# Kernel optimization log

Hardware: AMD Instinct MI355X
Metric: run time of the kernel (lower is better)

## Reference

```python
import jax, jax.numpy as jnp
import numpy as np

N_NODES = 50000
IN_CH, HID_CH, OUT_CH = 256, 128, 64
N_EDGES = 800000


def setup_inputs() -> dict:
    key = jax.random.key(0)
    ks = jax.random.split(key, 8)
    x = jax.random.normal(ks[0], (N_NODES, IN_CH), dtype=jnp.float32)
    edge_index = jax.random.randint(ks[1], (2, N_EDGES), 0, N_NODES, dtype=jnp.int64)
    edge_weight = jax.random.uniform(ks[2], (N_EDGES,), dtype=jnp.float32)
    # Glorot-style init for the two GCNConv linear layers (PyG uses glorot init, zero bias)
    W1 = jax.random.normal(ks[3], (IN_CH, HID_CH), dtype=jnp.float32) * (2.0 / (IN_CH + HID_CH)) ** 0.5
    b1 = jnp.zeros((HID_CH,), dtype=jnp.float32)
    W2 = jax.random.normal(ks[4], (HID_CH, OUT_CH), dtype=jnp.float32) * (2.0 / (HID_CH + OUT_CH)) ** 0.5
    b2 = jnp.zeros((OUT_CH,), dtype=jnp.float32)
    return {"x": x, "edge_index": edge_index, "edge_weight": edge_weight,
            "W1": W1, "b1": b1, "W2": W2, "b2": b2}


def _gcn_norm(edge_index, edge_weight, num_nodes):
    # PyG gcn_norm with add_self_loops=True: append self loops (weight 1.0),
    # deg[j] = sum of incoming edge weights, norm_e = deg[src]^-1/2 * w_e * deg[dst]^-1/2
    loop = jnp.arange(num_nodes, dtype=edge_index.dtype)
    row = jnp.concatenate([edge_index[0], loop])  # source nodes
    col = jnp.concatenate([edge_index[1], loop])  # destination nodes
    w = jnp.concatenate([edge_weight, jnp.ones((num_nodes,), dtype=edge_weight.dtype)])
    deg = jax.ops.segment_sum(w, col, num_segments=num_nodes)  # [N]
    deg_inv_sqrt = jnp.where(deg > 0, jax.lax.rsqrt(jnp.where(deg > 0, deg, 1.0)), 0.0)
    norm = deg_inv_sqrt[row] * w * deg_inv_sqrt[col]  # [E+N]
    return row, col, norm


def _gcn_conv(x, W, b, row, col, norm, num_nodes):
    h = x @ W                              # [N, C_out] dense linear first (as in PyG)
    msg = h[row] * norm[:, None]           # gather + per-edge scale: [E+N, C_out]
    out = jax.ops.segment_sum(msg, col, num_segments=num_nodes)  # scatter-add to dst
    return out + b


def reference(x, edge_index, edge_weight, W1, b1, W2, b2):
    num_nodes = x.shape[0]
    row, col, norm = _gcn_norm(edge_index, edge_weight, num_nodes)
    h = _gcn_conv(x, W1, b1, row, col, norm, num_nodes)
    h = jax.nn.relu(h)
    # dropout p=0.2 is identity in eval mode (training=False)
    out = _gcn_conv(h, W2, b2, row, col, norm, num_nodes)
    return out
```

## Files before the change

kernel.cpp:

```cpp
#include <hip/hip_runtime.h>
#include <hip/hip_bf16.h>
#include <math.h>

static constexpr int NNODES = 50000;
static constexpr int NEDGES = 800000;
static constexpr int NBUCK = (NNODES + 255) >> 8;
static constexpr int MAXB = 6144;

typedef __attribute__((ext_vector_type(8))) short bf16x8;
typedef __attribute__((ext_vector_type(4))) float f32x4;

__device__ inline short f2bf(float f) {
  union { __hip_bfloat16 h; short s; } u;
  u.h = __float2bfloat16(f);
  return u.s;
}

__device__ inline float bf2f(short s) {
  union { unsigned int u; float f; } u;
  u.u = ((unsigned int)(unsigned short)s) << 16;
  return u.f;
}

__device__ inline void i8x8_to_f32(uint2 v, float* f) {
#pragma unroll
  for (int j = 0; j < 4; ++j) f[j] = (float)(signed char)((v.x >> (8 * j)) & 0xFF);
#pragma unroll
  for (int j = 0; j < 4; ++j) f[4 + j] = (float)(signed char)((v.y >> (8 * j)) & 0xFF);
}


template <int K, int NTOT>
__device__ inline void packW_body(const float* __restrict__ W, short* __restrict__ Wpk, int t) {
  constexpr int KF = K / 32;
  constexpr int NPF = NTOT / 16;
  if (t >= KF * NPF * 64) return;
  int f = t >> 6, l = t & 63;
  int kf = f / NPF, nfb = f % NPF;
  int col = nfb * 16 + (l & 15);
  int krow = kf * 32 + (l >> 4) * 8;
  bf16x8 bv;
#pragma unroll
  for (int i = 0; i < 8; ++i) bv[i] = f2bf(W[(size_t)(krow + i) * NTOT + col]);
  ((bf16x8*)Wpk)[t] = bv;
}

__global__ void setup_kernel(const float* __restrict__ W1, short* __restrict__ Wpk1,
                             const float* __restrict__ W2, short* __restrict__ Wpk2,
                             int* __restrict__ gcur) {
  const int bid = blockIdx.x, tid = threadIdx.x;
  if (bid < 16) {
    packW_body<256, 128>(W1, Wpk1, bid * 256 + tid);
  } else if (bid < 20) {
    packW_body<128, 64>(W2, Wpk2, (bid - 16) * 256 + tid);
  } else {
    if (tid < NBUCK) gcur[tid] = tid * MAXB;
  }
}


__global__ __launch_bounds__(256) void bin_kernel(const int* __restrict__ row,
                                                  const int* __restrict__ col,
                                                  const float* __restrict__ w,
                                                  int* __restrict__ gcur,
                                                  int2* __restrict__ binned, int e_cnt) {
  __shared__ int rcnt[NBUCK];
  __shared__ int rcur[NBUCK];
  __shared__ int gbase[NBUCK];
  const int tid = threadIdx.x;
  for (int b = tid; b < NBUCK; b += 256) {
    rcnt[b] = 0;
    rcur[b] = 0;
  }
  __syncthreads();
  const int base = blockIdx.x * 2048;
  int srcs[8], dsts[8];
  float ws_[8];
#pragma unroll
  for (int j = 0; j < 8; ++j) {
    int idx = base + tid + 256 * j;
    if (idx < e_cnt) {
      srcs[j] = row[idx];
      dsts[j] = col[idx];
      ws_[j] = w[idx];
      atomicAdd(&rcnt[dsts[j] >> 8], 1);
    } else {
      dsts[j] = -1;
    }
  }
  __syncthreads();
  for (int b = tid; b < NBUCK; b += 256)
    if (rcnt[b] > 0) gbase[b] = atomicAdd(&gcur[b], rcnt[b]);
  __syncthreads();
#pragma unroll
  for (int j = 0; j < 8; ++j) {
    if (dsts[j] >= 0) {
      int b = dsts[j] >> 8;
      int dl = dsts[j] & 255;
      int pos = gbase[b] + atomicAdd(&rcur[b], 1);
      binned[pos] = make_int2((dl << 16) | srcs[j], __float_as_int(ws_[j]));
    }
  }
}

__global__ __launch_bounds__(256) void bdeg_kernel(const int2* __restrict__ binned,
                                                   const int* __restrict__ gcur,
                                                   float* __restrict__ dinv,
                                                   int* __restrict__ cntg,
                                                   int* __restrict__ bbase, int n) {
  const int b = blockIdx.x, tid = threadIdx.x;
  if (b == NBUCK) {
    __shared__ int buf[256];
    int v = (tid < NBUCK) ? gcur[tid] - tid * MAXB : 0;
    buf[tid] = v;
    __syncthreads();
    for (int off = 1; off < 256; off <<= 1) {
      int t = (tid >= off) ? buf[tid - off] : 0;
      __syncthreads();
      buf[tid] += t;
      __syncthreads();
    }
    if (tid < NBUCK) bbase[tid] = buf[tid] - v;
    return;
  }
  __shared__ float degf[256];
  __shared__ int cnt[256];
  degf[tid] = 0.f;
  cnt[tid] = 0;
  __syncthreads();
  const int bcnt = gcur[b] - b * MAXB;
  const int2* bp = binned + (size_t)b * MAXB;
  for (int i = tid; i < bcnt; i += 256) {
    int2 e = bp[i];
    int dl = (e.x >> 16) & 255;
    atomicAdd(&degf[dl], __int_as_float(e.y));
    atomicAdd(&cnt[dl], 1);
  }
  __syncthreads();
  int node = b * 256 + tid;
  if (node < n) {
    dinv[node] = 1.0f / sqrtf(degf[tid] + 1.0f);
    cntg[node] = cnt[tid];
  }
}

__global__ __launch_bounds__(256) void csrfill_kernel(
    const int2* __restrict__ binned, const int* __restrict__ gcur,
    const int* __restrict__ bbase, const float* __restrict__ dinv,
    const int* __restrict__ cntg, int* __restrict__ start,
    unsigned int* __restrict__ csr, int n) {
  __shared__ float dvL[256];
  __shared__ int cur[256];
  __shared__ int buf[256];
  const int b = blockIdx.x, tid = threadIdx.x;
  const int node = b * 256 + tid;
  int c = (node < n) ? cntg[node] : 0;
  dvL[tid] = (node < n) ? dinv[node] : 0.f;
  buf[tid] = c;
  __syncthreads();
  for (int off = 1; off < 256; off <<= 1) {
    int t = (tid >= off) ? buf[tid - off] : 0;
    __syncthreads();
    buf[tid] += t;
    __syncthreads();
  }
  int localstart = buf[tid] - c;
  const int gb = bbase[b];
  if (node < n) start[node] = gb + localstart;
  cur[tid] = localstart;
  __syncthreads();
  const int bcnt = gcur[b] - b * MAXB;
  const int2* bp = binned + (size_t)b * MAXB;
  for (int i = tid; i < bcnt; i += 256) {
    int2 e = bp[i];
    int src = e.x & 0xFFFF;
    int dl = (e.x >> 16) & 255;
    float nrm = dinv[src] * __int_as_float(e.y) * dvL[dl];
    int pos = gb + atomicAdd(&cur[dl], 1);
    csr[pos] = (unsigned int)src | ((unsigned int)(unsigned short)f2bf(nrm) << 16);
  }
}


template <int K, int NTOT, bool A_BF16>
__global__ __launch_bounds__(64, 4) void mfma_gemm_kernel(const void* __restrict__ Av,
                                                          const short* __restrict__ Wpk,
                                                          unsigned char* __restrict__ H,
                                                          float* __restrict__ sc, int n) {
  constexpr int KF = K / 32;
  constexpr int NF = NTOT / 16;
  const int lane = threadIdx.x;
  const int lrow = lane & 15;
  const int lgrp = lane >> 4;
  const int rowbase = blockIdx.x * 16;
  const int nmax = n - 1;
  int r = rowbase + lrow;
  r = r > nmax ? nmax : r;
  const bf16x8* Wf = (const bf16x8*)Wpk;
  f32x4 acc[NF] = {};

#pragma unroll
  for (int ks = 0; ks < KF; ++ks) {
    bf16x8 a;
    if (A_BF16) {
      const short* X = (const short*)Av;
      a = *(const bf16x8*)(X + (size_t)r * K + ks * 32 + lgrp * 8);
    } else {
      const float* X = (const float*)Av;
      const float* xp = X + (size_t)r * K + ks * 32 + lgrp * 8;
      float4 x0 = *(const float4*)xp;
      float4 x1 = *(const float4*)(xp + 4);
      a[0] = f2bf(x0.x);
      a[1] = f2bf(x0.y);
      a[2] = f2bf(x0.z);
      a[3] = f2bf(x0.w);
      a[4] = f2bf(x1.x);
      a[5] = f2bf(x1.y);
      a[6] = f2bf(x1.z);
      a[7] = f2bf(x1.w);
    }
#pragma unroll
    for (int nf = 0; nf < NF; ++nf) {
      bf16x8 bfr = Wf[(ks * NF + nf) * 64 + lane];
      acc[nf] = __builtin_amdgcn_mfma_f32_16x16x32_bf16(a, bfr, acc[nf], 0, 0, 0);
    }
  }

#pragma unroll
  for (int rr = 0; rr < 4; ++rr) {
    float m = 0.f;
#pragma unroll
    for (int nf = 0; nf < NF; ++nf) m = fmaxf(m, fabsf(acc[nf][rr]));
#pragma unroll
    for (int mask = 1; mask <= 8; mask <<= 1) m = fmaxf(m, __shfl_xor(m, mask));
    const int r2 = rowbase + lgrp * 4 + rr;
    const float inv = (m > 0.f) ? 127.f / m : 0.f;
    if (lrow == 0) sc[r2] = m * (1.f / 127.f);
#pragma unroll
    for (int nf = 0; nf < NF; ++nf) {
      int qv = (int)rintf(acc[nf][rr] * inv);
      qv = qv > 127 ? 127 : (qv < -127 ? -127 : qv);
      H[(size_t)r2 * NTOT + nf * 16 + lrow] = (unsigned char)(signed char)qv;
    }
  }
}


template <int CH, int TPN, bool RELU, bool OUT_BF16>
__global__ __launch_bounds__(256) void gatherq_kernel(
    const unsigned char* __restrict__ h, const float* __restrict__ sc,
    const float* __restrict__ dinv, const float* __restrict__ b,
    const int* __restrict__ start, const unsigned int* __restrict__ csr,
    void* __restrict__ outp, int n, int e_cnt) {
  constexpr int NPB = 256 / TPN;
  const int tid = threadIdx.x;
  const int q = tid % TPN;
  const int g = tid / TPN;
  const int d = blockIdx.x * NPB + g;
  if (d >= n) return;
  float s = dinv[d];
  s = s * s * sc[d];
  float f[8];
  i8x8_to_f32(*(const uint2*)(h + (size_t)d * CH + q * 8), f);
  float a0[8], a1[8], a2[8], a3[8];
#pragma unroll
  for (int j = 0; j < 8; ++j) {
    a0[j] = f[j] * s + b[q * 8 + j];
    a1[j] = 0.f;
    a2[j] = 0.f;
    a3[j] = 0.f;
  }
  const int k0 = start[d];
  const int k1 = (d + 1 < n) ? start[d + 1] : e_cnt;
  int k = k0;
  for (; k + 4 <= k1; k += 4) {
    unsigned int e0 = csr[k];
    unsigned int e1 = csr[k + 1];
    unsigned int e2 = csr[k + 2];
    unsigned int e3 = csr[k + 3];
    const int s0 = e0 & 0xFFFF, s1 = e1 & 0xFFFF, s2 = e2 & 0xFFFF, s3 = e3 & 0xFFFF;
    uint2 v0 = *(const uint2*)(h + (size_t)s0 * CH + q * 8);
    uint2 v1 = *(const uint2*)(h + (size_t)s1 * CH + q * 8);
    uint2 v2 = *(const uint2*)(h + (size_t)s2 * CH + q * 8);
    uint2 v3 = *(const uint2*)(h + (size_t)s3 * CH + q * 8);
    float n0 = bf2f((short)(e0 >> 16)) * sc[s0];
    float n1 = bf2f((short)(e1 >> 16)) * sc[s1];
    float n2 = bf2f((short)(e2 >> 16)) * sc[s2];
    float n3 = bf2f((short)(e3 >> 16)) * sc[s3];
    i8x8_to_f32(v0, f);
#pragma unroll
    for (int j = 0; j < 8; ++j) a0[j] += f[j] * n0;
    i8x8_to_f32(v1, f);
#pragma unroll
    for (int j = 0; j < 8; ++j) a1[j] += f[j] * n1;
    i8x8_to_f32(v2, f);
#pragma unroll
    for (int j = 0; j < 8; ++j) a2[j] += f[j] * n2;
    i8x8_to_f32(v3, f);
#pragma unroll
    for (int j = 0; j < 8; ++j) a3[j] += f[j] * n3;
  }
  for (; k < k1; ++k) {
    unsigned int e = csr[k];
    const int s0 = e & 0xFFFF;
    float nv = bf2f((short)(e >> 16)) * sc[s0];
    i8x8_to_f32(*(const uint2*)(h + (size_t)s0 * CH + q * 8), f);
#pragma unroll
    for (int j = 0; j < 8; ++j) a0[j] += f[j] * nv;
  }
#pragma unroll
  for (int j = 0; j < 8; ++j) a0[j] += (a1[j] + a2[j]) + a3[j];
  if (RELU) {
#pragma unroll
    for (int j = 0; j < 8; ++j) a0[j] = fmaxf(a0[j], 0.f);
  }
  if (OUT_BF16) {
    bf16x8 ov;
#pragma unroll
    for (int j = 0; j < 8; ++j) ov[j] = f2bf(a0[j]);
    *(bf16x8*)((short*)outp + (size_t)d * CH + q * 8) = ov;
  } else {
    float4* op = (float4*)outp + ((size_t)d * CH + q * 8) / 4;
    op[0] = make_float4(a0[0], a0[1], a0[2], a0[3]);
    op[1] = make_float4(a0[4], a0[5], a0[6], a0[7]);
  }
}


extern "C" void kernel_launch(void* const* d_in, const int* in_sizes, int n_in,
                              void* d_out, int out_size, void* d_ws, size_t ws_size,
                              hipStream_t stream) {
  const float* x = (const float*)d_in[0];
  const int* ei = (const int*)d_in[1];
  const float* ew = (const float*)d_in[2];
  const float* W1 = (const float*)d_in[3];
  const float* b1 = (const float*)d_in[4];
  const float* W2 = (const float*)d_in[5];
  const float* b2 = (const float*)d_in[6];
  float* outp = (float*)d_out;

  const int N = NNODES, E = NEDGES;
  const int* rowp = ei;
  const int* colp = ei + E;

  char* wsb = (char*)d_ws;
  int2* binned = (int2*)wsb;        wsb += (size_t)NBUCK * MAXB * 8;
  unsigned int* csr = (unsigned int*)wsb;  wsb += (size_t)E * 4;
  short* h1r = (short*)wsb;         wsb += (size_t)N * 128 * 2;
  unsigned char* h1 = (unsigned char*)wsb; wsb += (size_t)N * 128;
  unsigned char* h2 = (unsigned char*)wsb; wsb += (size_t)N * 64;
  short* Wpk1 = (short*)wsb;        wsb += (size_t)256 * 128 * 2;
  short* Wpk2 = (short*)wsb;        wsb += (size_t)128 * 64 * 2;
  float* sc1 = (float*)wsb;         wsb += (size_t)N * 4;
  float* sc2 = (float*)wsb;         wsb += (size_t)N * 4;
  float* dinv = (float*)wsb;        wsb += (size_t)N * 4;
  int* start = (int*)wsb;           wsb += (size_t)N * 4;
  int* cntg = (int*)wsb;            wsb += (size_t)N * 4;
  int* gcur = (int*)wsb;            wsb += (size_t)NBUCK * 4;
  int* bbase = (int*)wsb;           wsb += (size_t)NBUCK * 4;

  setup_kernel<<<21, 256, 0, stream>>>(W1, Wpk1, W2, Wpk2, gcur);

  bin_kernel<<<(E + 2047) / 2048, 256, 0, stream>>>(rowp, colp, ew, gcur, binned, E);
  bdeg_kernel<<<NBUCK + 1, 256, 0, stream>>>(binned, gcur, dinv, cntg, bbase, N);
  csrfill_kernel<<<NBUCK, 256, 0, stream>>>(binned, gcur, bbase, dinv, cntg, start, csr, N);

  mfma_gemm_kernel<256, 128, false><<<(N + 15) / 16, 64, 0, stream>>>(x, Wpk1, h1, sc1, N);
  gatherq_kernel<128, 16, true, true><<<(N + 15) / 16, 256, 0, stream>>>(
      h1, sc1, dinv, b1, start, csr, h1r, N, E);

  mfma_gemm_kernel<128, 64, true><<<(N + 15) / 16, 64, 0, stream>>>(h1r, Wpk2, h2, sc2, N);
  gatherq_kernel<64, 8, false, false><<<(N + 31) / 32, 256, 0, stream>>>(
      h2, sc2, dinv, b2, start, csr, outp, N, E);
}
```

Baseline: 108.2 us.

## Fuse first GEMM with edge binning into one heterogeneous kernel launch

Merges the layer-1 MFMA GEMM and the edge-binning pass into a single launch. Block IDs below a threshold run the GEMM, with four waves per block each handling 16 rows. The remaining blocks do binning, now processing 4096 edges per workgroup instead of 2048. This removes a launch and lets the independent GEMM and binning work run concurrently on the GPU. The cost is that the binning blocks reserve shared memory for bucket counters even on the GEMM path, and each binning thread holds more registers, which could lower occupancy.

```diff
diff --git a/kernel.cpp b/kernel.cpp
--- a/kernel.cpp
+++ b/kernel.cpp
@@ -6,6 +6,8 @@
 static constexpr int NEDGES = 800000;
 static constexpr int NBUCK = (NNODES + 255) >> 8;
 static constexpr int MAXB = 6144;
+static constexpr int GEMM1_BLKS = (NNODES + 63) / 64;
+static constexpr int BIN_WGS = (NEDGES + 4095) / 4096;
 
 typedef __attribute__((ext_vector_type(8))) short bf16x8;
 typedef __attribute__((ext_vector_type(4))) float f32x4;
@@ -59,25 +61,84 @@
 }
 
 
-__global__ __launch_bounds__(256) void bin_kernel(const int* __restrict__ row,
-                                                  const int* __restrict__ col,
-                                                  const float* __restrict__ w,
-                                                  int* __restrict__ gcur,
-                                                  int2* __restrict__ binned, int e_cnt) {
+__device__ inline void gemm1_wave(const float* __restrict__ X, const short* __restrict__ Wpk,
+                                  unsigned char* __restrict__ H, float* __restrict__ sc,
+                                  int n, int rowbase, int lane) {
+  constexpr int KF = 8;
+  constexpr int NF = 8;
+  const int lrow = lane & 15;
+  const int lgrp = lane >> 4;
+  const int nmax = n - 1;
+  int r = rowbase + lrow;
+  r = r > nmax ? nmax : r;
+  const bf16x8* Wf = (const bf16x8*)Wpk;
+  f32x4 acc[NF] = {};
+#pragma unroll
+  for (int ks = 0; ks < KF; ++ks) {
+    const float* xp = X + (size_t)r * 256 + ks * 32 + lgrp * 8;
+    float4 x0 = *(const float4*)xp;
+    float4 x1 = *(const float4*)(xp + 4);
+    bf16x8 a;
+    a[0] = f2bf(x0.x);
+    a[1] = f2bf(x0.y);
+    a[2] = f2bf(x0.z);
+    a[3] = f2bf(x0.w);
+    a[4] = f2bf(x1.x);
+    a[5] = f2bf(x1.y);
+    a[6] = f2bf(x1.z);
+    a[7] = f2bf(x1.w);
+#pragma unroll
+    for (int nf = 0; nf < NF; ++nf) {
+      bf16x8 bfr = Wf[(ks * NF + nf) * 64 + lane];
+      acc[nf] = __builtin_amdgcn_mfma_f32_16x16x32_bf16(a, bfr, acc[nf], 0, 0, 0);
+    }
+  }
+#pragma unroll
+  for (int rr = 0; rr < 4; ++rr) {
+    float m = 0.f;
+#pragma unroll
+    for (int nf = 0; nf < NF; ++nf) m = fmaxf(m, fabsf(acc[nf][rr]));
+#pragma unroll
+    for (int mask = 1; mask <= 8; mask <<= 1) m = fmaxf(m, __shfl_xor(m, mask));
+    const int r2 = rowbase + lgrp * 4 + rr;
+    const float inv = (m > 0.f) ? 127.f / m : 0.f;
+    if (r2 < n) {
+      if (lrow == 0) sc[r2] = m * (1.f / 127.f);
+#pragma unroll
+      for (int nf = 0; nf < NF; ++nf) {
+        int qv = (int)rintf(acc[nf][rr] * inv);
+        qv = qv > 127 ? 127 : (qv < -127 ? -127 : qv);
+        H[(size_t)r2 * 128 + nf * 16 + lrow] = (unsigned char)(signed char)qv;
+      }
+    }
+  }
+}
+
+__global__ __launch_bounds__(256) void fused1_kernel(
+    const float* __restrict__ x, const short* __restrict__ Wpk1,
+    unsigned char* __restrict__ h1, float* __restrict__ sc1, int n,
+    const int* __restrict__ row, const int* __restrict__ col, const float* __restrict__ w,
+    int* __restrict__ gcur, int2* __restrict__ binned, int e_cnt) {
   __shared__ int rcnt[NBUCK];
   __shared__ int rcur[NBUCK];
   __shared__ int gbase[NBUCK];
   const int tid = threadIdx.x;
+  if ((int)blockIdx.x < GEMM1_BLKS) {
+    const int rowbase = blockIdx.x * 64 + (tid >> 6) * 16;
+    gemm1_wave(x, Wpk1, h1, sc1, n, rowbase, tid & 63);
+    return;
+  }
+  const int wg = blockIdx.x - GEMM1_BLKS;
   for (int b = tid; b < NBUCK; b += 256) {
     rcnt[b] = 0;
     rcur[b] = 0;
   }
   __syncthreads();
-  const int base = blockIdx.x * 2048;
-  int srcs[8], dsts[8];
-  float ws_[8];
-#pragma unroll
-  for (int j = 0; j < 8; ++j) {
+  const int base = wg * 4096;
+  int srcs[16], dsts[16];
+  float ws_[16];
+#pragma unroll
+  for (int j = 0; j < 16; ++j) {
     int idx = base + tid + 256 * j;
     if (idx < e_cnt) {
       srcs[j] = row[idx];
@@ -93,7 +154,7 @@
     if (rcnt[b] > 0) gbase[b] = atomicAdd(&gcur[b], rcnt[b]);
   __syncthreads();
 #pragma unroll
-  for (int j = 0; j < 8; ++j) {
+  for (int j = 0; j < 16; ++j) {
     if (dsts[j] >= 0) {
       int b = dsts[j] >> 8;
       int dl = dsts[j] & 255;
@@ -102,6 +163,7 @@
     }
   }
 }
+
 
 __global__ __launch_bounds__(256) void bdeg_kernel(const int2* __restrict__ binned,
                                                    const int* __restrict__ gcur,
@@ -143,6 +205,7 @@
     cntg[node] = cnt[tid];
   }
 }
+
 
 __global__ __launch_bounds__(256) void csrfill_kernel(
     const int2* __restrict__ binned, const int* __restrict__ gcur,
@@ -361,11 +424,12 @@
 
   setup_kernel<<<21, 256, 0, stream>>>(W1, Wpk1, W2, Wpk2, gcur);
 
-  bin_kernel<<<(E + 2047) / 2048, 256, 0, stream>>>(rowp, colp, ew, gcur, binned, E);
+  fused1_kernel<<<GEMM1_BLKS + BIN_WGS, 256, 0, stream>>>(x, Wpk1, h1, sc1, N, rowp, colp,
+                                                          ew, gcur, binned, E);
+
   bdeg_kernel<<<NBUCK + 1, 256, 0, stream>>>(binned, gcur, dinv, cntg, bbase, N);
   csrfill_kernel<<<NBUCK, 256, 0, stream>>>(binned, gcur, bbase, dinv, cntg, start, csr, N);
 
-  mfma_gemm_kernel<256, 128, false><<<(N + 15) / 16, 64, 0, stream>>>(x, Wpk1, h1, sc1, N);
   gatherq_kernel<128, 16, true, true><<<(N + 15) / 16, 256, 0, stream>>>(
       h1, sc1, dinv, b1, start, csr, h1r, N, E);
 
```

After: 95.26 us. 1.14x faster.
